# Kernel optimization log

Measured on AMD Instinct MI355X. Metric: run time of the kernel, lower is better.

The kernel has to match this reference:

```python
import jax, jax.numpy as jnp
import numpy as np


def setup_inputs() -> dict:
    key = jax.random.key(0)
    ks = jax.random.split(key, 8)
    B, dz, K, N, dx, T = 64, 16, 16, 1024, 128, 500
    # initial latent state [n_trials, dz, k_particles]
    z0 = jax.random.normal(ks[0], (B, dz, K), jnp.float32)
    # per-latent leak/time-constant A = (1 - dt/tau), kept in (0.8, 0.99) for stability
    A = jax.random.uniform(ks[1], (dz,), jnp.float32, minval=0.8, maxval=0.99)
    # low-rank recurrent factors: n [dz, N] (right), m [N, dz] (left)
    n = jax.random.normal(ks[2], (dz, N), jnp.float32) * (1.0 / N)
    m = jax.random.normal(ks[3], (N, dz), jnp.float32) * (1.0 / np.sqrt(dz))
    # neuron bias h [N], latent bias hz [dz]
    h = jax.random.normal(ks[4], (N,), jnp.float32) * 0.1
    hz = jax.random.normal(ks[5], (dz,), jnp.float32) * 0.01
    # readout B [dz, dx] ~ sqrt(2/dy) randn, bias initialised to zero (as in Observation)
    Bobs = jax.random.normal(ks[6], (dz, dx), jnp.float32) * np.sqrt(2.0 / dz)
    Bias = jnp.zeros((dx,), jnp.float32)
    return {"z0": z0, "A": A, "n": n, "m": m, "h": h, "hz": hz,
            "Bobs": Bobs, "Bias": Bias, "T": T}


def reference(z0, A, n, m, h, hz, Bobs, Bias, T):
    """Low-rank RNN rolled out for T steps + linear (identity-nonlin) readout.

    Per step (Transition.forward with relu nonlinearity, weight_scaler=1, du=0):
        R   = relu(m @ z - h)                       # rates, [B, N, K]
        z'  = A * z + n @ R + hz                    # [B, dz, K]
    Readout (Observation.forward, identity nonlinearity):
        X = einsum('zx,bzTK->bxTK', Bobs, zs) + Bias
    """
    Ab = A[None, :, None]      # [1, dz, 1]
    hb = h[None, :, None]      # [1, N, 1]
    hzb = hz[None, :, None]    # [1, dz, 1]

    def step(z, _):
        X = jnp.einsum('Nz,bzk->bNk', m, z)           # project to neurons
        R = jax.nn.relu(X - hb)                       # rates
        z_new = Ab * z + jnp.einsum('zN,bNk->bzk', n, R) + hzb
        return z_new, z_new

    _, zs = jax.lax.scan(step, z0, None, length=T)    # [T, B, dz, K]
    zs = jnp.transpose(zs, (1, 2, 0, 3))              # [B, dz, T, K]
    # Observation readout
    X = jnp.einsum('zx,bzTK->bxTK', Bobs, zs) + Bias[None, :, None, None]
    return X
```

## Files before the change

### kernel.cpp

```cpp
#include <hip/hip_runtime.h>
#include <hip/hip_bf16.h>


typedef __attribute__((ext_vector_type(4))) short short4v;
typedef __attribute__((ext_vector_type(8))) short short8v;
typedef __attribute__((ext_vector_type(4))) float float4v;

#define BB 64
#define DZ 16
#define KC 16
#define NN 1024
#define DX 128
#define NW 8
#define ITER (NN / (16 * NW))
#define NH (ITER / 2)
#define CH 16

#define BARRIER_LGKM() asm volatile("s_waitcnt lgkmcnt(0)\n\ts_barrier" ::: "memory")

union FragAB {
  short4v s;
  __hip_bfloat162 h2[2];
};
union Frag8 {
  short8v s8;
  short4v s4[2];
};

__device__ inline short4v pack_bf16x4(float a, float b, float c, float d) {
  FragAB u;
  u.h2[0] = __float22bfloat162_rn(make_float2(a, b));
  u.h2[1] = __float22bfloat162_rn(make_float2(c, d));
  return u.s;
}

__device__ inline float4v mfma_bf16(short4v a, short4v b, float4v c) {
#if __has_builtin(__builtin_amdgcn_mfma_f32_16x16x16bf16_1k)
  return __builtin_amdgcn_mfma_f32_16x16x16bf16_1k(a, b, c, 0, 0, 0);
#else
  float4v d;
  asm("v_mfma_f32_16x16x16_bf16 %0, %1, %2, %3"
      : "=v"(d) : "v"(a), "v"(b), "v"(c));
  return d;
#endif
}

__device__ inline float4v mfma_bf16_x32(short8v a, short8v b, float4v c) {
#if __has_builtin(__builtin_amdgcn_mfma_f32_16x16x32_bf16)
  return __builtin_amdgcn_mfma_f32_16x16x32_bf16(a, b, c, 0, 0, 0);
#else
  float4v d;
  asm("v_mfma_f32_16x16x32_bf16 %0, %1, %2, %3"
      : "=v"(d) : "v"(a), "v"(b), "v"(c));
  return d;
#endif
}

__global__ __launch_bounds__(64 * NW, 2)
void lrrnn_fused(const float* __restrict__ z0, const float* __restrict__ Adec,
                 const float* __restrict__ nmat, const float* __restrict__ mmat,
                 const float* __restrict__ hvec, const float* __restrict__ hzvec,
                 const float* __restrict__ Bobs, const float* __restrict__ Bias,
                 const int* __restrict__ Tptr, float* __restrict__ out)
{
  const int T    = Tptr[0];
  const int b    = blockIdx.x;
  const int tid  = threadIdx.x;
  const int wave = tid >> 6;
  const int lane = tid & 63;
  const int g    = lane >> 4;
  const int c    = lane & 15;

  __shared__ float4v part[NW][64];
  __shared__ short4v zbuf[64];

  FragAB mf[ITER];
  Frag8  nf8[NH];
  float4v negH[ITER];
#pragma unroll
  for (int i = 0; i < ITER; ++i) {
    const int rowbase = wave * (16 * ITER) + i * 16;
    float4v mv = *(const float4v*)(mmat + (rowbase + c) * DZ + g * 4);
    mf[i].s = pack_bf16x4(mv[0], mv[1], mv[2], mv[3]);
    float4v hv = *(const float4v*)(hvec + rowbase + g * 4);
    negH[i][0] = -hv[0]; negH[i][1] = -hv[1];
    negH[i][2] = -hv[2]; negH[i][3] = -hv[3];
  }
#pragma unroll
  for (int i = 0; i < NH; ++i) {
    const int rb0 = wave * (16 * ITER) + (2 * i) * 16;
    float4v nv0 = *(const float4v*)(nmat + c * NN + rb0 + g * 4);
    float4v nv1 = *(const float4v*)(nmat + c * NN + rb0 + 16 + g * 4);
    nf8[i].s4[0] = pack_bf16x4(nv0[0], nv0[1], nv0[2], nv0[3]);
    nf8[i].s4[1] = pack_bf16x4(nv1[0], nv1[1], nv1[2], nv1[3]);
  }

  const float4v Af  = *(const float4v*)(Adec + g * 4);
  const float4v hzf = *(const float4v*)(hzvec + g * 4);
  const float4v zerov = {0.f, 0.f, 0.f, 0.f};

  FragAB bobsF;
  float4v biasF;
  unsigned oof[4];
  {
    const int xb = wave * 16;
    bobsF.s = pack_bf16x4(Bobs[(4 * g + 0) * DX + xb + c],
                          Bobs[(4 * g + 1) * DX + xb + c],
                          Bobs[(4 * g + 2) * DX + xb + c],
                          Bobs[(4 * g + 3) * DX + xb + c]);
    biasF = *(const float4v*)(Bias + xb + g * 4);
#pragma unroll
    for (int rr = 0; rr < 4; ++rr) {
      const int x = xb + g * 4 + rr;
      oof[rr] = (unsigned)(b * DX + x) * (unsigned)T * KC + c;
    }
  }

  float4v zf;
#pragma unroll
  for (int j = 0; j < 4; ++j)
    zf[j] = z0[b * DZ * KC + (g * 4 + j) * KC + c];
  FragAB zb;
  zb.s = pack_bf16x4(zf[0], zf[1], zf[2], zf[3]);

  auto do_step = [&]() {
    float4v xv[ITER];
#pragma unroll
    for (int i = 0; i < ITER; ++i)
      xv[i] = mfma_bf16(mf[i].s, zb.s, negH[i]);

    Frag8 R8[NH];
#pragma unroll
    for (int i = 0; i < NH; ++i) {
      const float4v x0 = xv[2 * i], x1 = xv[2 * i + 1];
      R8[i].s4[0] = pack_bf16x4(fmaxf(x0[0], 0.f), fmaxf(x0[1], 0.f),
                                fmaxf(x0[2], 0.f), fmaxf(x0[3], 0.f));
      R8[i].s4[1] = pack_bf16x4(fmaxf(x1[0], 0.f), fmaxf(x1[1], 0.f),
                                fmaxf(x1[2], 0.f), fmaxf(x1[3], 0.f));
    }

    float4v a0 = mfma_bf16_x32(nf8[0].s8, R8[0].s8, (wave == 0) ? hzf : zerov);
    float4v a1 = mfma_bf16_x32(nf8[1].s8, R8[1].s8, zerov);
    a0 = mfma_bf16_x32(nf8[2].s8, R8[2].s8, a0);
    a1 = mfma_bf16_x32(nf8[3].s8, R8[3].s8, a1);
    const float4v zp = a0 + a1;

    part[wave][lane] = zp;
    BARRIER_LGKM();

    if (wave == 0) {
      const float4v p1 = part[1][lane];
      const float4v p2 = part[2][lane];
      const float4v p3 = part[3][lane];
      const float4v p4 = part[4][lane];
      const float4v p5 = part[5][lane];
      const float4v p6 = part[6][lane];
      const float4v p7 = part[7][lane];
      const float4v tot = ((zp + p1) + (p2 + p3)) + ((p4 + p5) + (p6 + p7));
#pragma unroll
      for (int j = 0; j < 4; ++j)
        zf[j] = fmaf(Af[j], zf[j], tot[j]);
      zb.s = pack_bf16x4(zf[0], zf[1], zf[2], zf[3]);
      zbuf[lane] = zb.s;
    }
    BARRIER_LGKM();

    if (wave != 0) zb.s = zbuf[lane];
  };

  int t = 0;
  while (t + CH <= T) {
    short4v hist[CH];
#pragma unroll
    for (int s = 0; s < CH; ++s) {
      do_step();
      hist[s] = zb.s;
    }
#pragma unroll
    for (int s = 0; s < CH; ++s) {
      float4v o = mfma_bf16(bobsF.s, hist[s], biasF);
      const unsigned tk = (unsigned)(t + s) * KC;
#pragma unroll
      for (int rr = 0; rr < 4; ++rr)
        out[oof[rr] + tk] = o[rr];
    }
    t += CH;
  }
  for (; t < T; ++t) {
    do_step();
    float4v o = mfma_bf16(bobsF.s, zb.s, biasF);
    const unsigned tk = (unsigned)t * KC;
#pragma unroll
    for (int rr = 0; rr < 4; ++rr)
      out[oof[rr] + tk] = o[rr];
  }
}

extern "C" void kernel_launch(void* const* d_in, const int* in_sizes, int n_in,
                              void* d_out, int out_size, void* d_ws, size_t ws_size,
                              hipStream_t stream) {
  const float* z0   = (const float*)d_in[0];
  const float* A    = (const float*)d_in[1];
  const float* nmat = (const float*)d_in[2];
  const float* mmat = (const float*)d_in[3];
  const float* h    = (const float*)d_in[4];
  const float* hz   = (const float*)d_in[5];
  const float* Bobs = (const float*)d_in[6];
  const float* Bias = (const float*)d_in[7];
  const int*   T    = (const int*)d_in[8];
  (void)in_sizes; (void)n_in; (void)out_size; (void)d_ws; (void)ws_size;
  lrrnn_fused<<<dim3(BB), dim3(64 * NW), 0, stream>>>(
      z0, A, nmat, mmat, h, hz, Bobs, Bias, T, (float*)d_out);
}
```

Measured before the change: 342.8 us.

## Overlap readout with wave-0 reduction by assigning output tiles to waves 1-7

```diff
diff --git a/kernel.cpp b/kernel.cpp
--- a/kernel.cpp
+++ b/kernel.cpp
@@ -14,7 +14,6 @@
 #define NW 8
 #define ITER (NN / (16 * NW))
 #define NH (ITER / 2)
-#define CH 16
 
 #define BARRIER_LGKM() asm volatile("s_waitcnt lgkmcnt(0)\n\ts_barrier" ::: "memory")
 
@@ -99,20 +98,24 @@
   const float4v hzf = *(const float4v*)(hzvec + g * 4);
   const float4v zerov = {0.f, 0.f, 0.f, 0.f};
 
-  FragAB bobsF;
-  float4v biasF;
-  unsigned oof[4];
-  {
-    const int xb = wave * 16;
-    bobsF.s = pack_bf16x4(Bobs[(4 * g + 0) * DX + xb + c],
-                          Bobs[(4 * g + 1) * DX + xb + c],
-                          Bobs[(4 * g + 2) * DX + xb + c],
-                          Bobs[(4 * g + 3) * DX + xb + c]);
-    biasF = *(const float4v*)(Bias + xb + g * 4);
+  const int t0 = (wave >= 1) ? (wave - 1) : 0;
+  const int nt = (wave == 1) ? 2 : ((wave == 0) ? 0 : 1);
+  int tiles[2] = {t0, 7};
+  FragAB bobsF[2];
+  float4v biasF[2];
+  unsigned oof[2][4];
+#pragma unroll
+  for (int s = 0; s < 2; ++s) {
+    const int xb = tiles[s] * 16;
+    bobsF[s].s = pack_bf16x4(Bobs[(4 * g + 0) * DX + xb + c],
+                             Bobs[(4 * g + 1) * DX + xb + c],
+                             Bobs[(4 * g + 2) * DX + xb + c],
+                             Bobs[(4 * g + 3) * DX + xb + c]);
+    biasF[s] = *(const float4v*)(Bias + xb + g * 4);
 #pragma unroll
     for (int rr = 0; rr < 4; ++rr) {
       const int x = xb + g * 4 + rr;
-      oof[rr] = (unsigned)(b * DX + x) * (unsigned)T * KC + c;
+      oof[s][rr] = (unsigned)(b * DX + x) * (unsigned)T * KC + c;
     }
   }
 
@@ -123,7 +126,7 @@
   FragAB zb;
   zb.s = pack_bf16x4(zf[0], zf[1], zf[2], zf[3]);
 
-  auto do_step = [&]() {
+  for (int t = 0; t < T; ++t) {
     float4v xv[ITER];
 #pragma unroll
     for (int i = 0; i < ITER; ++i)
@@ -145,7 +148,7 @@
     a1 = mfma_bf16_x32(nf8[3].s8, R8[3].s8, a1);
     const float4v zp = a0 + a1;
 
-    part[wave][lane] = zp;
+    if (wave != 0) part[wave][lane] = zp;
     BARRIER_LGKM();
 
     if (wave == 0) {
@@ -162,37 +165,34 @@
         zf[j] = fmaf(Af[j], zf[j], tot[j]);
       zb.s = pack_bf16x4(zf[0], zf[1], zf[2], zf[3]);
       zbuf[lane] = zb.s;
+    } else if (t > 0) {
+      const unsigned tk = (unsigned)(t - 1) * KC;
+#pragma unroll
+      for (int s = 0; s < 2; ++s) {
+        if (s < nt) {
+          float4v o = mfma_bf16(bobsF[s].s, zb.s, biasF[s]);
+#pragma unroll
+          for (int rr = 0; rr < 4; ++rr)
+            out[oof[s][rr] + tk] = o[rr];
+        }
+      }
     }
     BARRIER_LGKM();
 
     if (wave != 0) zb.s = zbuf[lane];
-  };
-
-  int t = 0;
-  while (t + CH <= T) {
-    short4v hist[CH];
-#pragma unroll
-    for (int s = 0; s < CH; ++s) {
-      do_step();
-      hist[s] = zb.s;
-    }
-#pragma unroll
-    for (int s = 0; s < CH; ++s) {
-      float4v o = mfma_bf16(bobsF.s, hist[s], biasF);
-      const unsigned tk = (unsigned)(t + s) * KC;
-#pragma unroll
-      for (int rr = 0; rr < 4; ++rr)
-        out[oof[rr] + tk] = o[rr];
-    }
-    t += CH;
-  }
-  for (; t < T; ++t) {
-    do_step();
-    float4v o = mfma_bf16(bobsF.s, zb.s, biasF);
-    const unsigned tk = (unsigned)t * KC;
-#pragma unroll
-    for (int rr = 0; rr < 4; ++rr)
-      out[oof[rr] + tk] = o[rr];
+  }
+
+  if (wave != 0) {
+    const unsigned tk = (unsigned)(T - 1) * KC;
+#pragma unroll
+    for (int s = 0; s < 2; ++s) {
+      if (s < nt) {
+        float4v o = mfma_bf16(bobsF[s].s, zb.s, biasF[s]);
+#pragma unroll
+        for (int rr = 0; rr < 4; ++rr)
+          out[oof[s][rr] + tk] = o[rr];
+      }
+    }
   }
 }
 
```

Result: no change. 341.5 us (-0.4%).
